# Performance work log

Hardware: AMD Instinct MI355X
Metric: run time of the kernel (lower is better)

The kernel has to match this reference:

```python
import jax, jax.numpy as jnp
import numpy as np

D_MODEL = 512
CONTEXT_LENGTH = 128


def setup_inputs() -> dict:
    key = jax.random.key(0)
    k1, k2, k3, k4 = jax.random.split(key, 4)
    B, T, C = 512, 128, D_MODEL
    H = 64  # head_size
    x = jax.random.normal(k1, (B, T, C), dtype=jnp.float32)
    # torch nn.Linear(d_model, head_size, bias=False) stores weight as [head_size, d_model]
    s = 1.0 / np.sqrt(C)
    Wq = jax.random.uniform(k2, (H, C), dtype=jnp.float32, minval=-s, maxval=s)
    Wk = jax.random.uniform(k3, (H, C), dtype=jnp.float32, minval=-s, maxval=s)
    Wv = jax.random.uniform(k4, (H, C), dtype=jnp.float32, minval=-s, maxval=s)
    return {"x": x, "Wq": Wq, "Wk": Wk, "Wv": Wv}


def reference(x, Wq, Wk, Wv):
    # x: [B, T, C]; Wq/Wk/Wv: [H, C] (torch Linear weight layout, y = x @ W^T)
    B, T, C = x.shape
    H = Wq.shape[0]
    Q = jnp.einsum('btc,hc->bth', x, Wq)  # [B, T, H]
    K = jnp.einsum('btc,hc->bth', x, Wk)
    V = jnp.einsum('btc,hc->bth', x, Wv)
    scale = 1.0 / jnp.sqrt(jnp.asarray(H, dtype=x.dtype))
    scores = jnp.einsum('bth,bsh->bts', Q, K) * scale  # [B, T, T]
    causal = jnp.tril(jnp.ones((T, T), dtype=bool))
    scores = jnp.where(causal, scores, jnp.asarray(-jnp.inf, dtype=scores.dtype))
    weights = jax.nn.softmax(scores, axis=-1)
    # dropout is identity in eval mode (reference baseline)
    out = jnp.einsum('bts,bsh->bth', weights, V)  # [B, T, H]
    return out
```

## Files before the change

kernel.cpp:

```cpp
#include <hip/hip_runtime.h>
#include <hip/hip_bf16.h>


#define TT 128
#define CC 512
#define HH 64

typedef __attribute__((ext_vector_type(8))) short bf16x8;
typedef __attribute__((ext_vector_type(4))) float f32x4;

__device__ __forceinline__ ushort f2bf(float f) {
    union { float f; unsigned u; } v; v.f = f;
    unsigned r = v.u + 0x7fffu + ((v.u >> 16) & 1u);
    return (ushort)(r >> 16);
}

__device__ __forceinline__ void gload_lds16(const void* g, void* l) {
    __builtin_amdgcn_global_load_lds(
        (const __attribute__((address_space(1))) unsigned int*)g,
        (__attribute__((address_space(3))) unsigned int*)l, 16, 0, 0);
}

__global__ void wpack_kernel(const float* __restrict__ wq,
                             const float* __restrict__ wk,
                             const float* __restrict__ wv,
                             ushort* __restrict__ wpk) {
    int p = blockIdx.x * 256 + threadIdx.x;
    int j  = p & 7;
    int l  = (p >> 3) & 63;
    int nt = (p >> 9) % 12;
    int kt = p / (12 * 512);
    int w  = nt >> 2;
    const float* src = (w == 0) ? wq : ((w == 1) ? wk : wv);
    int h = (nt & 3) * 16 + (l & 15);
    int c = kt * 32 + ((l >> 4) << 3) + j;
    wpk[kt * 8192 + ((nt * 64 + l) * 8) + j] = f2bf(src[h * 512 + c]);
}

__launch_bounds__(512, 4)
__global__ void attn_fused_kernel(const float* __restrict__ x,
                                  const ushort* __restrict__ wpk,
                                  float* __restrict__ out) {
    __shared__ __align__(16) char smem[65536];
    ushort* qs  = (ushort*)smem;
    ushort* ks  = (ushort*)(smem + 16384);
    ushort* vst = (ushort*)(smem + 32768);
    ushort* ps  = (ushort*)smem;

    const int tid  = threadIdx.x;
    const int wave = tid >> 6;
    const int lane = tid & 63;
    const int lq   = lane >> 4;
    const int lr   = lane & 15;
    const int b    = blockIdx.x;
    const size_t bB = (size_t)b * TT;

    const f32x4 fzero = {0.f, 0.f, 0.f, 0.f};

    f32x4 acc[12];
    #pragma unroll
    for (int j = 0; j < 12; ++j) acc[j] = fzero;

    auto stage = [&](int kt, int s) {
        const char* wsrc = (const char*)(wpk + kt * 8192);
        char* wdst = smem + s * 16384;
        #pragma unroll
        for (int p = 0; p < 2; ++p) {
            int off = wave * 2048 + p * 1024;
            gload_lds16(wsrc + off + lane * 16, wdst + off);
        }
        char* xdst = smem + 32768 + s * 16384;
        #pragma unroll
        for (int p = 0; p < 2; ++p) {
            int uoff = wave * 2048 + p * 1024;
            int off  = uoff + lane * 16;
            int row  = off >> 7;
            int slot = (off >> 4) & 7;
            int g    = slot ^ (row & 7);
            const float* src = x + (bB + row) * CC + kt * 32 + g * 4;
            gload_lds16(src, xdst + uoff);
        }
    };

    stage(0, 0);

    const int r = wave * 16 + lr;
    for (int kt = 0; kt < 16; ++kt) {
        const int cur = kt & 1;

        __builtin_amdgcn_s_barrier();

        if (kt + 1 < 16) {
            stage(kt + 1, cur ^ 1);
            asm volatile("s_waitcnt vmcnt(4)" ::: "memory");
        } else {
            asm volatile("s_waitcnt vmcnt(0)" ::: "memory");
        }
        __builtin_amdgcn_sched_barrier(0);

        __builtin_amdgcn_s_barrier();
        __builtin_amdgcn_sched_barrier(0);

        const float* xs = (const float*)(smem + 32768 + cur * 16384);
        int s0 = (lq * 2) ^ (r & 7);
        int s1 = (lq * 2 + 1) ^ (r & 7);
        f32x4 alo = *(const f32x4*)(xs + r * 32 + s0 * 4);
        f32x4 ahi = *(const f32x4*)(xs + r * 32 + s1 * 4);

        const ushort* wf = (const ushort*)(smem + cur * 16384);
        bf16x8 w[12];
        #pragma unroll
        for (int nt = 0; nt < 12; ++nt)
            w[nt] = *(const bf16x8*)(wf + (nt * 64 + lane) * 8);

        bf16x8 a;
        a[0] = (short)f2bf(alo[0]); a[1] = (short)f2bf(alo[1]);
        a[2] = (short)f2bf(alo[2]); a[3] = (short)f2bf(alo[3]);
        a[4] = (short)f2bf(ahi[0]); a[5] = (short)f2bf(ahi[1]);
        a[6] = (short)f2bf(ahi[2]); a[7] = (short)f2bf(ahi[3]);

        #pragma unroll
        for (int nt = 0; nt < 12; ++nt)
            acc[nt] = __builtin_amdgcn_mfma_f32_16x16x32_bf16(a, w[nt], acc[nt], 0, 0, 0);
    }

    __syncthreads();

    #pragma unroll
    for (int nt = 0; nt < 12; ++nt)
        #pragma unroll
        for (int j = 0; j < 4; ++j) {
            int t = wave * 16 + lq * 4 + j;
            int h = (nt & 3) * 16 + lr;
            ushort v = f2bf(acc[nt][j]);
            if (nt < 4)      qs[t * 64 + (h ^ ((t & 7) << 3))] = v;
            else if (nt < 8) ks[t * 64 + (h ^ ((t & 7) << 3))] = v;
            else             vst[h * 128 + (t ^ ((h & 7) << 3))] = v;
        }
    __syncthreads();

    const int row0 = wave * 16;
    f32x4 s[8];
    #pragma unroll
    for (int j = 0; j < 8; ++j) s[j] = fzero;

    #pragma unroll
    for (int kt = 0; kt < 2; ++kt) {
        int h0 = kt * 32 + lq * 8;
        int t  = row0 + lr;
        bf16x8 a = *(const bf16x8*)&qs[t * 64 + (h0 ^ ((t & 7) << 3))];
        bf16x8 kf[8];
        #pragma unroll
        for (int nt = 0; nt < 8; ++nt) {
            int sc = nt * 16 + lr;
            kf[nt] = *(const bf16x8*)&ks[sc * 64 + (h0 ^ ((sc & 7) << 3))];
        }
        #pragma unroll
        for (int nt = 0; nt < 8; ++nt)
            s[nt] = __builtin_amdgcn_mfma_f32_16x16x32_bf16(a, kf[nt], s[nt], 0, 0, 0);
    }

    float rinv[4];
    #pragma unroll
    for (int j = 0; j < 4; ++j) {
        int t = row0 + lq * 4 + j;
        float m = -1e30f;
        #pragma unroll
        for (int nt = 0; nt < 8; ++nt) {
            int sc = nt * 16 + lr;
            float v = s[nt][j] * 0.125f;
            v = (sc <= t) ? v : -1e30f;
            s[nt][j] = v;
            m = fmaxf(m, v);
        }
        m = fmaxf(m, __shfl_xor(m, 1));
        m = fmaxf(m, __shfl_xor(m, 2));
        m = fmaxf(m, __shfl_xor(m, 4));
        m = fmaxf(m, __shfl_xor(m, 8));
        float sum = 0.f;
        #pragma unroll
        for (int nt = 0; nt < 8; ++nt) {
            float p = __expf(s[nt][j] - m);
            s[nt][j] = p;
            sum += p;
        }
        sum += __shfl_xor(sum, 1);
        sum += __shfl_xor(sum, 2);
        sum += __shfl_xor(sum, 4);
        sum += __shfl_xor(sum, 8);
        rinv[j] = 1.0f / sum;
    }

    __syncthreads();

    #pragma unroll
    for (int j = 0; j < 4; ++j) {
        int t = row0 + lq * 4 + j;
        #pragma unroll
        for (int nt = 0; nt < 8; ++nt) {
            int sc = nt * 16 + lr;
            ps[t * 128 + (sc ^ ((t & 7) << 3))] = f2bf(s[nt][j]);
        }
    }
    __syncthreads();

    f32x4 o[4];
    #pragma unroll
    for (int j = 0; j < 4; ++j) o[j] = fzero;

    #pragma unroll
    for (int ksv = 0; ksv < 4; ++ksv) {
        int s0 = ksv * 32 + lq * 8;
        int t  = row0 + lr;
        bf16x8 a = *(const bf16x8*)&ps[t * 128 + (s0 ^ ((t & 7) << 3))];
        bf16x8 vf[4];
        #pragma unroll
        for (int nt = 0; nt < 4; ++nt) {
            int h = nt * 16 + lr;
            vf[nt] = *(const bf16x8*)&vst[h * 128 + (s0 ^ ((h & 7) << 3))];
        }
        #pragma unroll
        for (int nt = 0; nt < 4; ++nt)
            o[nt] = __builtin_amdgcn_mfma_f32_16x16x32_bf16(a, vf[nt], o[nt], 0, 0, 0);
    }

    float* ob = out + (size_t)b * (TT * HH);
    #pragma unroll
    for (int nt = 0; nt < 4; ++nt)
        #pragma unroll
        for (int j = 0; j < 4; ++j) {
            int t = row0 + lq * 4 + j;
            int h = nt * 16 + lr;
            ob[t * HH + h] = o[nt][j] * rinv[j];
        }
}

extern "C" void kernel_launch(void* const* d_in, const int* in_sizes, int n_in,
                              void* d_out, int out_size, void* d_ws, size_t ws_size,
                              hipStream_t stream) {
    const float* x  = (const float*)d_in[0];
    const float* wq = (const float*)d_in[1];
    const float* wk = (const float*)d_in[2];
    const float* wv = (const float*)d_in[3];
    float* o = (float*)d_out;
    ushort* wpk = (ushort*)d_ws;

    (void)in_sizes; (void)n_in; (void)out_size; (void)ws_size;

    wpack_kernel<<<384, 256, 0, stream>>>(wq, wk, wv, wpk);
    attn_fused_kernel<<<512, 512, 0, stream>>>(x, wpk, o);
}
```

Measured before the change: 38.84 us.

## Load x directly into registers and double K-step per stage in projection GEMM

The projection loop now loads x rows straight from global memory into registers with inline-asm dwordx4 loads, prefetched two stages ahead. Previously x was staged through LDS. Each stage now covers 64 channels (two MFMA k-steps), so there are 8 iterations instead of 16 and half as many barriers. Only the packed weights still go through double-buffered LDS, which cuts shared memory from 64KB to 48KB and may allow more resident blocks. The trade-offs are hand-tuned vmcnt counts that must exactly match the issued loads, and higher register pressure from holding two x buffers.

```diff
diff --git a/kernel.cpp b/kernel.cpp
--- a/kernel.cpp
+++ b/kernel.cpp
@@ -13,6 +13,15 @@
     union { float f; unsigned u; } v; v.f = f;
     unsigned r = v.u + 0x7fffu + ((v.u >> 16) & 1u);
     return (ushort)(r >> 16);
+}
+
+__device__ __forceinline__ bf16x8 pack8(f32x4 lo, f32x4 hi) {
+    bf16x8 a;
+    a[0] = (short)f2bf(lo[0]); a[1] = (short)f2bf(lo[1]);
+    a[2] = (short)f2bf(lo[2]); a[3] = (short)f2bf(lo[3]);
+    a[4] = (short)f2bf(hi[0]); a[5] = (short)f2bf(hi[1]);
+    a[6] = (short)f2bf(hi[2]); a[7] = (short)f2bf(hi[3]);
+    return a;
 }
 
 __device__ __forceinline__ void gload_lds16(const void* g, void* l) {
@@ -29,21 +38,21 @@
     int j  = p & 7;
     int l  = (p >> 3) & 63;
     int nt = (p >> 9) % 12;
-    int kt = p / (12 * 512);
+    int ks = p / (12 * 512);
     int w  = nt >> 2;
     const float* src = (w == 0) ? wq : ((w == 1) ? wk : wv);
     int h = (nt & 3) * 16 + (l & 15);
-    int c = kt * 32 + ((l >> 4) << 3) + j;
-    wpk[kt * 8192 + ((nt * 64 + l) * 8) + j] = f2bf(src[h * 512 + c]);
+    int c = ks * 32 + ((l >> 4) << 3) + j;
+    wpk[p] = f2bf(src[h * 512 + c]);
 }
 
 __launch_bounds__(512, 4)
 __global__ void attn_fused_kernel(const float* __restrict__ x,
                                   const ushort* __restrict__ wpk,
                                   float* __restrict__ out) {
-    __shared__ __align__(16) char smem[65536];
+    __shared__ __align__(16) char smem[49152];
     ushort* qs  = (ushort*)smem;
-    ushort* ks  = (ushort*)(smem + 16384);
+    ushort* ksm = (ushort*)(smem + 16384);
     ushort* vst = (ushort*)(smem + 32768);
     ushort* ps  = (ushort*)smem;
 
@@ -61,67 +70,76 @@
     #pragma unroll
     for (int j = 0; j < 12; ++j) acc[j] = fzero;
 
-    auto stage = [&](int kt, int s) {
-        const char* wsrc = (const char*)(wpk + kt * 8192);
-        char* wdst = smem + s * 16384;
-        #pragma unroll
-        for (int p = 0; p < 2; ++p) {
-            int off = wave * 2048 + p * 1024;
+    const int r = wave * 16 + lr;
+    const float* xr = x + (bB + r) * CC + lq * 8;
+
+    auto stageW = [&](int kt, int s) {
+        const char* wsrc = (const char*)wpk + kt * 24576;
+        char* wdst = smem + s * 24576;
+        #pragma unroll
+        for (int p = 0; p < 3; ++p) {
+            int off = wave * 3072 + p * 1024;
             gload_lds16(wsrc + off + lane * 16, wdst + off);
         }
-        char* xdst = smem + 32768 + s * 16384;
-        #pragma unroll
-        for (int p = 0; p < 2; ++p) {
-            int uoff = wave * 2048 + p * 1024;
-            int off  = uoff + lane * 16;
-            int row  = off >> 7;
-            int slot = (off >> 4) & 7;
-            int g    = slot ^ (row & 7);
-            const float* src = x + (bB + row) * CC + kt * 32 + g * 4;
-            gload_lds16(src, xdst + uoff);
-        }
     };
 
-    stage(0, 0);
-
-    const int r = wave * 16 + lr;
-    for (int kt = 0; kt < 16; ++kt) {
+    #define LOADX(kt, d0, d1, d2, d3)                                          \
+        {                                                                      \
+            const float* p0 = xr + (kt) * 64;                                  \
+            asm volatile("global_load_dwordx4 %0, %1, off"                     \
+                         : "=&v"(d0) : "v"(p0) : "memory");                    \
+            asm volatile("global_load_dwordx4 %0, %1, off offset:16"           \
+                         : "=&v"(d1) : "v"(p0) : "memory");                    \
+            asm volatile("global_load_dwordx4 %0, %1, off offset:128"          \
+                         : "=&v"(d2) : "v"(p0) : "memory");                    \
+            asm volatile("global_load_dwordx4 %0, %1, off offset:144"          \
+                         : "=&v"(d3) : "v"(p0) : "memory");                    \
+        }
+
+    f32x4 xA0, xA1, xA2, xA3, xB0, xB1, xB2, xB3;
+
+    stageW(0, 0);
+    LOADX(0, xA0, xA1, xA2, xA3);
+    LOADX(1, xB0, xB1, xB2, xB3);
+
+    #pragma unroll
+    for (int kt = 0; kt < 8; ++kt) {
         const int cur = kt & 1;
 
         __builtin_amdgcn_s_barrier();
 
-        if (kt + 1 < 16) {
-            stage(kt + 1, cur ^ 1);
-            asm volatile("s_waitcnt vmcnt(4)" ::: "memory");
-        } else {
-            asm volatile("s_waitcnt vmcnt(0)" ::: "memory");
-        }
+        if (kt == 0)      asm volatile("s_waitcnt vmcnt(4)" ::: "memory");
+        else if (kt == 7) asm volatile("s_waitcnt vmcnt(3)" ::: "memory");
+        else              asm volatile("s_waitcnt vmcnt(7)" ::: "memory");
         __builtin_amdgcn_sched_barrier(0);
 
+        bf16x8 a0, a1;
+        if (cur == 0) { a0 = pack8(xA0, xA1); a1 = pack8(xA2, xA3); }
+        else          { a0 = pack8(xB0, xB1); a1 = pack8(xB2, xB3); }
+
+        if (kt + 1 < 8) stageW(kt + 1, cur ^ 1);
+        if (kt + 2 < 8) {
+            if (cur == 0) LOADX(kt + 2, xA0, xA1, xA2, xA3)
+            else          LOADX(kt + 2, xB0, xB1, xB2, xB3)
+        }
+
+        if (kt <= 5)      asm volatile("s_waitcnt vmcnt(11)" ::: "memory");
+        else if (kt == 6) asm volatile("s_waitcnt vmcnt(7)" ::: "memory");
+        else              asm volatile("s_waitcnt vmcnt(0)" ::: "memory");
+        __builtin_amdgcn_sched_barrier(0);
         __builtin_amdgcn_s_barrier();
         __builtin_amdgcn_sched_barrier(0);
 
-        const float* xs = (const float*)(smem + 32768 + cur * 16384);
-        int s0 = (lq * 2) ^ (r & 7);
-        int s1 = (lq * 2 + 1) ^ (r & 7);
-        f32x4 alo = *(const f32x4*)(xs + r * 32 + s0 * 4);
-        f32x4 ahi = *(const f32x4*)(xs + r * 32 + s1 * 4);
-
-        const ushort* wf = (const ushort*)(smem + cur * 16384);
-        bf16x8 w[12];
-        #pragma unroll
-        for (int nt = 0; nt < 12; ++nt)
-            w[nt] = *(const bf16x8*)(wf + (nt * 64 + lane) * 8);
-
-        bf16x8 a;
-        a[0] = (short)f2bf(alo[0]); a[1] = (short)f2bf(alo[1]);
-        a[2] = (short)f2bf(alo[2]); a[3] = (short)f2bf(alo[3]);
-        a[4] = (short)f2bf(ahi[0]); a[5] = (short)f2bf(ahi[1]);
-        a[6] = (short)f2bf(ahi[2]); a[7] = (short)f2bf(ahi[3]);
-
-        #pragma unroll
-        for (int nt = 0; nt < 12; ++nt)
-            acc[nt] = __builtin_amdgcn_mfma_f32_16x16x32_bf16(a, w[nt], acc[nt], 0, 0, 0);
+        const ushort* wf = (const ushort*)(smem + cur * 24576);
+        #pragma unroll
+        for (int kh = 0; kh < 2; ++kh) {
+            bf16x8 a = kh ? a1 : a0;
+            #pragma unroll
+            for (int nt = 0; nt < 12; ++nt) {
+                bf16x8 bb = *(const bf16x8*)(wf + kh * 6144 + (nt * 64 + lane) * 8);
+                acc[nt] = __builtin_amdgcn_mfma_f32_16x16x32_bf16(a, bb, acc[nt], 0, 0, 0);
+            }
+        }
     }
 
     __syncthreads();
@@ -134,7 +152,7 @@
             int h = (nt & 3) * 16 + lr;
             ushort v = f2bf(acc[nt][j]);
             if (nt < 4)      qs[t * 64 + (h ^ ((t & 7) << 3))] = v;
-            else if (nt < 8) ks[t * 64 + (h ^ ((t & 7) << 3))] = v;
+            else if (nt < 8) ksm[t * 64 + (h ^ ((t & 7) << 3))] = v;
             else             vst[h * 128 + (t ^ ((h & 7) << 3))] = v;
         }
     __syncthreads();
@@ -153,7 +171,7 @@
         #pragma unroll
         for (int nt = 0; nt < 8; ++nt) {
             int sc = nt * 16 + lr;
-            kf[nt] = *(const bf16x8*)&ks[sc * 64 + (h0 ^ ((sc & 7) << 3))];
+            kf[nt] = *(const bf16x8*)&ksm[sc * 64 + (h0 ^ ((sc & 7) << 3))];
         }
         #pragma unroll
         for (int nt = 0; nt < 8; ++nt)
```

New measurement: 40.27 us. 3.7% more time.

## Load x directly into registers and triple-buffer weight tiles in LDS

Applied to the files above, without the earlier changes.

The projection loop no longer stages x through LDS. Each lane now loads its own x fragment straight into registers with inline global_load_dwordx4. Weight tiles are triple-buffered with a prefetch distance of two, and the LDS footprint drops from 64KB to 48KB. The loop is fully unrolled, and weight fragment reads are interleaved with MFMAs in groups of four. The aim is to hide global latency better and cut LDS traffic. The cost is more registers and hand-tuned vmcnt waits, which could be wrong if the compiler reorders loads.

```diff
diff --git a/kernel.cpp b/kernel.cpp
--- a/kernel.cpp
+++ b/kernel.cpp
@@ -41,7 +41,7 @@
 __global__ void attn_fused_kernel(const float* __restrict__ x,
                                   const ushort* __restrict__ wpk,
                                   float* __restrict__ out) {
-    __shared__ __align__(16) char smem[65536];
+    __shared__ __align__(16) char smem[49152];
     ushort* qs  = (ushort*)smem;
     ushort* ks  = (ushort*)(smem + 16384);
     ushort* vst = (ushort*)(smem + 32768);
@@ -61,67 +61,80 @@
     #pragma unroll
     for (int j = 0; j < 12; ++j) acc[j] = fzero;
 
-    auto stage = [&](int kt, int s) {
-        const char* wsrc = (const char*)(wpk + kt * 8192);
+    const int r = wave * 16 + lr;
+    const float* xr = x + (bB + r) * CC + lq * 8;
+
+    auto stageW = [&](int kt, int s) {
+        const char* wsrc = (const char*)wpk + kt * 16384;
         char* wdst = smem + s * 16384;
         #pragma unroll
         for (int p = 0; p < 2; ++p) {
             int off = wave * 2048 + p * 1024;
             gload_lds16(wsrc + off + lane * 16, wdst + off);
         }
-        char* xdst = smem + 32768 + s * 16384;
-        #pragma unroll
-        for (int p = 0; p < 2; ++p) {
-            int uoff = wave * 2048 + p * 1024;
-            int off  = uoff + lane * 16;
-            int row  = off >> 7;
-            int slot = (off >> 4) & 7;
-            int g    = slot ^ (row & 7);
-            const float* src = x + (bB + row) * CC + kt * 32 + g * 4;
-            gload_lds16(src, xdst + uoff);
-        }
     };
 
-    stage(0, 0);
-
-    const int r = wave * 16 + lr;
+    #define LOADX(kt, dlo, dhi)                                                \
+        {                                                                      \
+            const float* p0 = xr + (kt) * 32;                                  \
+            asm volatile("global_load_dwordx4 %0, %1, off"                     \
+                         : "=&v"(dlo) : "v"(p0) : "memory");                   \
+            asm volatile("global_load_dwordx4 %0, %1, off offset:16"           \
+                         : "=&v"(dhi) : "v"(p0) : "memory");                   \
+        }
+
+    f32x4 x0a, x0b, x1a, x1b, x2a, x2b;
+
+    stageW(0, 0);
+    stageW(1, 1);
+    LOADX(0, x0a, x0b);
+    LOADX(1, x1a, x1b);
+
+    #pragma unroll
     for (int kt = 0; kt < 16; ++kt) {
-        const int cur = kt & 1;
+        const int cur = kt % 3;
 
         __builtin_amdgcn_s_barrier();
 
-        if (kt + 1 < 16) {
-            stage(kt + 1, cur ^ 1);
-            asm volatile("s_waitcnt vmcnt(4)" ::: "memory");
-        } else {
-            asm volatile("s_waitcnt vmcnt(0)" ::: "memory");
-        }
+        if (kt + 2 < 16) {
+            stageW(kt + 2, (kt + 2) % 3);
+            const int slot = (kt + 2) % 3;
+            if (slot == 0)      LOADX(kt + 2, x0a, x0b)
+            else if (slot == 1) LOADX(kt + 2, x1a, x1b)
+            else                LOADX(kt + 2, x2a, x2b)
+        }
+
+        if (kt == 0)       asm volatile("s_waitcnt vmcnt(6)" ::: "memory");
+        else if (kt <= 13) asm volatile("s_waitcnt vmcnt(8)" ::: "memory");
+        else if (kt == 14) asm volatile("s_waitcnt vmcnt(4)" ::: "memory");
+        else               asm volatile("s_waitcnt vmcnt(0)" ::: "memory");
         __builtin_amdgcn_sched_barrier(0);
 
         __builtin_amdgcn_s_barrier();
         __builtin_amdgcn_sched_barrier(0);
 
-        const float* xs = (const float*)(smem + 32768 + cur * 16384);
-        int s0 = (lq * 2) ^ (r & 7);
-        int s1 = (lq * 2 + 1) ^ (r & 7);
-        f32x4 alo = *(const f32x4*)(xs + r * 32 + s0 * 4);
-        f32x4 ahi = *(const f32x4*)(xs + r * 32 + s1 * 4);
-
-        const ushort* wf = (const ushort*)(smem + cur * 16384);
-        bf16x8 w[12];
-        #pragma unroll
-        for (int nt = 0; nt < 12; ++nt)
-            w[nt] = *(const bf16x8*)(wf + (nt * 64 + lane) * 8);
-
+        f32x4 alo, ahi;
+        if (cur == 0)      { alo = x0a; ahi = x0b; }
+        else if (cur == 1) { alo = x1a; ahi = x1b; }
+        else               { alo = x2a; ahi = x2b; }
         bf16x8 a;
         a[0] = (short)f2bf(alo[0]); a[1] = (short)f2bf(alo[1]);
         a[2] = (short)f2bf(alo[2]); a[3] = (short)f2bf(alo[3]);
         a[4] = (short)f2bf(ahi[0]); a[5] = (short)f2bf(ahi[1]);
         a[6] = (short)f2bf(ahi[2]); a[7] = (short)f2bf(ahi[3]);
 
-        #pragma unroll
-        for (int nt = 0; nt < 12; ++nt)
-            acc[nt] = __builtin_amdgcn_mfma_f32_16x16x32_bf16(a, w[nt], acc[nt], 0, 0, 0);
+        const ushort* wf = (const ushort*)(smem + cur * 16384);
+        #pragma unroll
+        for (int g = 0; g < 3; ++g) {
+            bf16x8 w0 = *(const bf16x8*)(wf + ((g * 4 + 0) * 64 + lane) * 8);
+            bf16x8 w1 = *(const bf16x8*)(wf + ((g * 4 + 1) * 64 + lane) * 8);
+            bf16x8 w2 = *(const bf16x8*)(wf + ((g * 4 + 2) * 64 + lane) * 8);
+            bf16x8 w3 = *(const bf16x8*)(wf + ((g * 4 + 3) * 64 + lane) * 8);
+            acc[g * 4 + 0] = __builtin_amdgcn_mfma_f32_16x16x32_bf16(a, w0, acc[g * 4 + 0], 0, 0, 0);
+            acc[g * 4 + 1] = __builtin_amdgcn_mfma_f32_16x16x32_bf16(a, w1, acc[g * 4 + 1], 0, 0, 0);
+            acc[g * 4 + 2] = __builtin_amdgcn_mfma_f32_16x16x32_bf16(a, w2, acc[g * 4 + 2], 0, 0, 0);
+            acc[g * 4 + 3] = __builtin_amdgcn_mfma_f32_16x16x32_bf16(a, w3, acc[g * 4 + 3], 0, 0, 0);
+        }
     }
 
     __syncthreads();
```

After: 39.39 us. Within noise of the previous version (+1.4%).
